# Kernel tuning notes

Hardware: AMD Instinct MI355X
Metric: run time of the kernel (lower is better)

Reference implementation:

```python
import jax, jax.numpy as jnp
import numpy as np

B, H, SQ, SK, D, INT, F = 1, 32, 2048, 2048, 128, 128, 32
THOLD = 0.5


def _mlp(x, W1, b1, W2, b2, W3, b3):
    # x: [b,h,s,d]; W*: [h,out,in] (torch Linear layout), y = x @ W^T + b, per head
    h = jax.nn.silu(jnp.einsum('bhsd,hid->bhsi', x, W1) + b1[None, :, None, :])
    h = jax.nn.silu(jnp.einsum('bhsi,hji->bhsj', h, W2) + b2[None, :, None, :])
    return jnp.einsum('bhsj,hfj->bhsf', h, W3) + b3[None, :, None, :]


def setup_inputs() -> dict:
    key = jax.random.key(0)
    ks = jax.random.split(key, 16)
    sc = 0.05  # small init so tanh stays in its linear-ish range
    inp = {
        'K': jax.random.normal(ks[0], (B, H, SK, D), jnp.float32),
        'Q': jax.random.normal(ks[1], (B, H, SQ, D), jnp.float32),
        'Wk1': jax.random.normal(ks[2], (H, INT, D), jnp.float32) * sc,
        'bk1': jax.random.normal(ks[3], (H, INT), jnp.float32) * sc,
        'Wk2': jax.random.normal(ks[4], (H, INT, INT), jnp.float32) * sc,
        'bk2': jax.random.normal(ks[5], (H, INT), jnp.float32) * sc,
        'Wk3': jax.random.normal(ks[6], (H, F, INT), jnp.float32) * sc,
        'bk3': jax.random.normal(ks[7], (H, F), jnp.float32) * sc,
        'Wq1': jax.random.normal(ks[8], (H, INT, D), jnp.float32) * sc,
        'bq1': jax.random.normal(ks[9], (H, INT), jnp.float32) * sc,
        'Wq2': jax.random.normal(ks[10], (H, INT, INT), jnp.float32) * sc,
        'bq2': jax.random.normal(ks[11], (H, INT), jnp.float32) * sc,
        'Wq3': jax.random.normal(ks[12], (H, F, INT), jnp.float32) * sc,
        'bq3': jax.random.normal(ks[13], (H, F), jnp.float32) * sc,
    }
    return inp


def reference(K, Q, Wk1, bk1, Wk2, bk2, Wk3, bk3, Wq1, bq1, Wq2, bq2, Wq3, bq3):
    # soft (hard=False) path of USA.forward
    Kl = jnp.tanh(_mlp(K, Wk1, bk1, Wk2, bk2, Wk3, bk3))  # [b,h,sk,F]
    Ql = jnp.tanh(_mlp(Q, Wq1, bq1, Wq2, bq2, Wq3, bq3))  # [b,h,sq,F]
    scores = jnp.einsum('bhtf,bhsf->bhts', Ql, Kl)        # [b,h,sq,sk]
    sq, sk = Q.shape[2], K.shape[2]
    causal = jnp.tril(jnp.ones((sq, sk), dtype=bool), k=sk - sq)
    mask_val = jnp.asarray(jnp.finfo(scores.dtype).min, scores.dtype)
    scores = jnp.where(causal[None, None], scores, mask_val)
    return jax.nn.sigmoid(scores - THOLD)
```

## Files before the change

### kernel.cpp

```cpp
#include <hip/hip_runtime.h>

#define NH  32
#define SEQ 2048
#define DIM 128
#define FD  32

typedef short          short8 __attribute__((ext_vector_type(8)));
typedef float          f32x4  __attribute__((ext_vector_type(4)));
typedef unsigned short u16x8  __attribute__((ext_vector_type(8)));

static __device__ __forceinline__ unsigned short f2bf(float f) {
    unsigned int u = __builtin_bit_cast(unsigned int, f);
    u += 0x7fffu + ((u >> 16) & 1u);
    return (unsigned short)(u >> 16);
}
static __device__ __forceinline__ float fexp(float x) {
    return __builtin_amdgcn_exp2f(x * 1.44269504088896f);
}
static __device__ __forceinline__ float sigm(float x) {
    return __builtin_amdgcn_rcpf(1.0f + fexp(-x));
}
static __device__ __forceinline__ float silu_f(float x) { return x * sigm(x); }
static __device__ __forceinline__ float tanh_f(float x) {
    return 1.0f - 2.0f * __builtin_amdgcn_rcpf(fexp(2.0f * x) + 1.0f);
}

#define WPH 36864
#define WPS (32 * WPH)

__global__ __launch_bounds__(256) void prep_weights(
    const float* __restrict__ Wk1, const float* __restrict__ Wk2,
    const float* __restrict__ Wk3, const float* __restrict__ Wq1,
    const float* __restrict__ Wq2, const float* __restrict__ Wq3,
    unsigned short* __restrict__ wimg) {
    int c = blockIdx.x * 256 + threadIdx.x;
    int s = (c >= 147456) ? 1 : 0;
    c -= s * 147456;
    const float* src;
    int dst;
    int sB = s * WPS;
    if (c < 65536) {
        int h = c >> 11, idx = c & 2047;
        int r = idx >> 4, jb = (idx & 15) * 8;
        src = (s ? Wq1 : Wk1) + h * 16384 + r * 128 + jb;
        dst = sB + h * WPH + r * 128 + (jb ^ ((r & 7) << 3));
    } else if (c < 131072) {
        int cc = c - 65536;
        int h = cc >> 11, idx = cc & 2047;
        int r = idx >> 4, jb = (idx & 15) * 8;
        src = (s ? Wq2 : Wk2) + h * 16384 + r * 128 + jb;
        dst = sB + h * WPH + 16384 + r * 128 + (jb ^ ((r & 7) << 3));
    } else {
        int cc = c - 131072;
        int h = cc >> 9, idx = cc & 511;
        int r = idx >> 4, jb = (idx & 15) * 8;
        src = (s ? Wq3 : Wk3) + h * 4096 + r * 128 + jb;
        dst = sB + h * WPH + 32768 + r * 128 + (jb ^ ((r & 7) << 3));
    }
    f32x4 u0 = *(const f32x4*)src;
    f32x4 u1 = *(const f32x4*)(src + 4);
    u16x8 p;
    p[0] = f2bf(u0[0]); p[1] = f2bf(u0[1]); p[2] = f2bf(u0[2]); p[3] = f2bf(u0[3]);
    p[4] = f2bf(u1[0]); p[5] = f2bf(u1[1]); p[6] = f2bf(u1[2]); p[7] = f2bf(u1[3]);
    *(u16x8*)(&wimg[dst]) = p;
}

template <int OT, int ACT, bool LIN>
static __device__ __forceinline__ void compute_layer(
    const short8 a[4], const unsigned short* W,
    const float* __restrict__ bias, unsigned short* dst, int lane, int wid) {
    int r0 = lane & 15, q = lane >> 4, kb = q * 8;
#pragma unroll
    for (int ot = 0; ot < OT; ++ot) {
        int wrow = ot * 16 + r0;
        int sw   = (wrow & 7) << 3;
        short8 b[4];
#pragma unroll
        for (int ks = 0; ks < 4; ++ks)
            b[ks] = *(const short8*)(&W[wrow * 128 + ((ks * 32 + kb) ^ sw)]);
        f32x4 acc = {0.f, 0.f, 0.f, 0.f};
#pragma unroll
        for (int ks = 0; ks < 4; ++ks)
            acc = __builtin_amdgcn_mfma_f32_16x16x32_bf16(a[ks], b[ks], acc, 0, 0, 0);
        float bv = bias[wrow];
#pragma unroll
        for (int r = 0; r < 4; ++r) {
            float y = acc[r] + bv;
            float v = (ACT == 0) ? silu_f(y) : tanh_f(y);
            int orow = wid * 16 + q * 4 + r;
            int ocol = ot * 16 + r0;
            if (LIN)
                dst[orow * FD + ocol] = f2bf(v);
            else
                dst[orow * 128 + (ocol ^ ((orow & 7) << 3))] = f2bf(v);
        }
    }
}

__global__ __launch_bounds__(256) void mlp_kernel(
    const float* __restrict__ K,  const float* __restrict__ Q,
    const float* __restrict__ bk1, const float* __restrict__ bk2,
    const float* __restrict__ bk3, const float* __restrict__ bq1,
    const float* __restrict__ bq2, const float* __restrict__ bq3,
    const unsigned short* __restrict__ wimg,
    unsigned short* __restrict__ Kl, unsigned short* __restrict__ Ql) {
    __shared__ unsigned short wb[128 * 128];
    __shared__ unsigned short w3[32 * 128];
    __shared__ unsigned short act[64 * 128];
    __shared__ unsigned short outb[64 * FD];
    int raw = blockIdx.x;
    int bid = (raw & 7) * 256 + (raw >> 3);
    int tb  = bid & 31;
    int h   = (bid >> 5) & 31;
    int s   = bid >> 10;

    const float* X  = s ? Q : K;
    const unsigned short* Wb = wimg + s * WPS + h * WPH;
    const float* B1 = (s ? bq1 : bk1) + h * 128;
    const float* B2 = (s ? bq2 : bk2) + h * 128;
    const float* B3 = (s ? bq3 : bk3) + h * FD;
    unsigned short* gout = (s ? Ql : Kl) + ((size_t)h * SEQ + (size_t)tb * 64) * FD;

    int tid = threadIdx.x, lane = tid & 63, wid = tid >> 6;
    int r0 = lane & 15, kb = (lane >> 4) * 8;

    const u16x8* wsrc = (const u16x8*)Wb;
#pragma unroll
    for (int i = 0; i < 8; ++i)
        *(u16x8*)(&wb[(i * 256 + tid) * 8]) = wsrc[i * 256 + tid];
    const u16x8* w3src = (const u16x8*)(Wb + 32768);
#pragma unroll
    for (int i = 0; i < 2; ++i)
        *(u16x8*)(&w3[(i * 256 + tid) * 8]) = w3src[i * 256 + tid];

    short8 a[4];
    const float* xs = X + ((size_t)h * SEQ + (size_t)tb * 64) * DIM;
    int row = wid * 16 + r0;
#pragma unroll
    for (int ks = 0; ks < 4; ++ks) {
        const float* p = xs + row * 128 + ks * 32 + kb;
        f32x4 u0 = *(const f32x4*)p;
        f32x4 u1 = *(const f32x4*)(p + 4);
        short8 t;
        t[0] = f2bf(u0[0]); t[1] = f2bf(u0[1]); t[2] = f2bf(u0[2]); t[3] = f2bf(u0[3]);
        t[4] = f2bf(u1[0]); t[5] = f2bf(u1[1]); t[6] = f2bf(u1[2]); t[7] = f2bf(u1[3]);
        a[ks] = t;
    }
    __syncthreads();
    compute_layer<8, 0, false>(a, wb, B1, act, lane, wid);
    __syncthreads();
#pragma unroll
    for (int i = 0; i < 8; ++i)
        *(u16x8*)(&wb[(i * 256 + tid) * 8]) = wsrc[2048 + i * 256 + tid];
    __syncthreads();
    {
        int sw = (row & 7) << 3;
#pragma unroll
        for (int ks = 0; ks < 4; ++ks)
            a[ks] = *(const short8*)(&act[row * 128 + ((ks * 32 + kb) ^ sw)]);
    }
    compute_layer<8, 0, false>(a, wb, B2, act, lane, wid);
    {
        int sw = (row & 7) << 3;
#pragma unroll
        for (int ks = 0; ks < 4; ++ks)
            a[ks] = *(const short8*)(&act[row * 128 + ((ks * 32 + kb) ^ sw)]);
    }
    compute_layer<2, 1, true>(a, w3, B3, outb, lane, wid);
    __syncthreads();
    *(u16x8*)(gout + tid * 8) = *(const u16x8*)(&outb[tid * 8]);
}

__global__ __launch_bounds__(256) void score_kernel(
    const unsigned short* __restrict__ Ql, const unsigned short* __restrict__ Kl,
    float* __restrict__ out) {
    int bid = blockIdx.x;
    int h   = bid >> 8;
    int tr  = (bid >> 4) & 15;
    int tc  = bid & 15;
    int tq0 = tr * 128, tk0 = tc * 128;
    int tid = threadIdx.x;
    float* ob = out + (size_t)h * SEQ * SEQ;

    if (tc > tr) {
        f32x4 z = {0.f, 0.f, 0.f, 0.f};
        for (int it = 0; it < 16; ++it) {
            int row = tq0 + it * 8 + (tid >> 5);
            int c0  = tk0 + (tid & 31) * 4;
            *(f32x4*)(ob + (size_t)row * SEQ + c0) = z;
        }
        return;
    }
    bool diag = (tc == tr);
    __shared__ float sb[4][16 * 68];
    int lane = tid & 63;
    int wid  = tid >> 6;
    int tqw  = tq0 + (wid >> 1) * 64;
    int tkw  = tk0 + (wid & 1) * 64;
    int kb   = (lane >> 4) * 8;

    short8 aq[4], bk[4];
#pragma unroll
    for (int i = 0; i < 4; ++i) {
        aq[i] = *(const short8*)(Ql + ((size_t)h * SEQ + tqw + i * 16 + (lane & 15)) * FD + kb);
        bk[i] = *(const short8*)(Kl + ((size_t)h * SEQ + tkw + i * 16 + (lane & 15)) * FD + kb);
    }
    float* my = sb[wid];
#pragma unroll
    for (int qr = 0; qr < 4; ++qr) {
#pragma unroll
        for (int ct = 0; ct < 4; ++ct) {
            f32x4 acc = {0.f, 0.f, 0.f, 0.f};
            acc = __builtin_amdgcn_mfma_f32_16x16x32_bf16(aq[qr], bk[ct], acc, 0, 0, 0);
#pragma unroll
            for (int r = 0; r < 4; ++r) {
                int lr  = (lane >> 4) * 4 + r;
                int col = ct * 16 + (lane & 15);
                float o = sigm(acc[r] - 0.5f);
                if (diag && (tkw + col) > (tqw + qr * 16 + lr)) o = 0.0f;
                my[lr * 68 + col] = o;
            }
        }
#pragma unroll
        for (int it = 0; it < 2; ++it) {
            int lr = it * 8 + (lane >> 3);
            int c0 = (lane & 7) * 8;
            f32x4 v0 = *(const f32x4*)(&my[lr * 68 + c0]);
            f32x4 v1 = *(const f32x4*)(&my[lr * 68 + c0 + 4]);
            float* dst = ob + (size_t)(tqw + qr * 16 + lr) * SEQ + tkw + c0;
            *(f32x4*)dst       = v0;
            *(f32x4*)(dst + 4) = v1;
        }
    }
}

extern "C" void kernel_launch(void* const* d_in, const int* in_sizes, int n_in,
                              void* d_out, int out_size, void* d_ws, size_t ws_size,
                              hipStream_t stream) {
    const float* K   = (const float*)d_in[0];
    const float* Q   = (const float*)d_in[1];
    const float* Wk1 = (const float*)d_in[2];
    const float* bk1 = (const float*)d_in[3];
    const float* Wk2 = (const float*)d_in[4];
    const float* bk2 = (const float*)d_in[5];
    const float* Wk3 = (const float*)d_in[6];
    const float* bk3 = (const float*)d_in[7];
    const float* Wq1 = (const float*)d_in[8];
    const float* bq1 = (const float*)d_in[9];
    const float* Wq2 = (const float*)d_in[10];
    const float* bq2 = (const float*)d_in[11];
    const float* Wq3 = (const float*)d_in[12];
    const float* bq3 = (const float*)d_in[13];

    unsigned short* Kl   = (unsigned short*)d_ws;
    unsigned short* Ql   = Kl + (size_t)NH * SEQ * FD;
    unsigned short* wimg = Ql + (size_t)NH * SEQ * FD;

    prep_weights<<<dim3(1152), dim3(256), 0, stream>>>(
        Wk1, Wk2, Wk3, Wq1, Wq2, Wq3, wimg);

    mlp_kernel<<<dim3(2 * NH * (SEQ / 64)), dim3(256), 0, stream>>>(
        K, Q, bk1, bk2, bk3, bq1, bq2, bq3, wimg, Kl, Ql);

    score_kernel<<<dim3(NH * 16 * 16), dim3(256), 0, stream>>>(
        Ql, Kl, (float*)d_out);
}
```

Before: 155.9 us.

## Hold layer-3 weights in registers; stage full-width score rows per block

Measured after the change: 139.9 us. 10.3% less time.

```diff
diff --git a/kernel.cpp b/kernel.cpp
--- a/kernel.cpp
+++ b/kernel.cpp
@@ -65,7 +65,7 @@
     *(u16x8*)(&wimg[dst]) = p;
 }
 
-template <int OT, int ACT, bool LIN>
+template <int OT, int ACT>
 static __device__ __forceinline__ void compute_layer(
     const short8 a[4], const unsigned short* W,
     const float* __restrict__ bias, unsigned short* dst, int lane, int wid) {
@@ -89,10 +89,26 @@
             float v = (ACT == 0) ? silu_f(y) : tanh_f(y);
             int orow = wid * 16 + q * 4 + r;
             int ocol = ot * 16 + r0;
-            if (LIN)
-                dst[orow * FD + ocol] = f2bf(v);
-            else
-                dst[orow * 128 + (ocol ^ ((orow & 7) << 3))] = f2bf(v);
+            dst[orow * 128 + (ocol ^ ((orow & 7) << 3))] = f2bf(v);
+        }
+    }
+}
+
+static __device__ __forceinline__ void compute_layer3_reg(
+    const short8 a[4], const short8 w3f[2][4],
+    const float* __restrict__ bias, unsigned short* dst, int lane, int wid) {
+    int r0 = lane & 15, q = lane >> 4;
+#pragma unroll
+    for (int ot = 0; ot < 2; ++ot) {
+        f32x4 acc = {0.f, 0.f, 0.f, 0.f};
+#pragma unroll
+        for (int ks = 0; ks < 4; ++ks)
+            acc = __builtin_amdgcn_mfma_f32_16x16x32_bf16(a[ks], w3f[ot][ks], acc, 0, 0, 0);
+        float bv = bias[ot * 16 + r0];
+#pragma unroll
+        for (int r = 0; r < 4; ++r) {
+            float v = tanh_f(acc[r] + bv);
+            dst[(wid * 16 + q * 4 + r) * FD + ot * 16 + r0] = f2bf(v);
         }
     }
 }
@@ -105,7 +121,6 @@
     const unsigned short* __restrict__ wimg,
     unsigned short* __restrict__ Kl, unsigned short* __restrict__ Ql) {
     __shared__ unsigned short wb[128 * 128];
-    __shared__ unsigned short w3[32 * 128];
     __shared__ unsigned short act[64 * 128];
     __shared__ unsigned short outb[64 * FD];
     int raw = blockIdx.x;
@@ -124,14 +139,21 @@
     int tid = threadIdx.x, lane = tid & 63, wid = tid >> 6;
     int r0 = lane & 15, kb = (lane >> 4) * 8;
 
+    short8 w3f[2][4];
+    {
+        const unsigned short* W3g = Wb + 32768;
+        int sw = (r0 & 7) << 3;
+#pragma unroll
+        for (int ot = 0; ot < 2; ++ot)
+#pragma unroll
+            for (int ks = 0; ks < 4; ++ks)
+                w3f[ot][ks] = *(const short8*)(&W3g[(ot * 16 + r0) * 128 + ((ks * 32 + kb) ^ sw)]);
+    }
+
     const u16x8* wsrc = (const u16x8*)Wb;
 #pragma unroll
     for (int i = 0; i < 8; ++i)
         *(u16x8*)(&wb[(i * 256 + tid) * 8]) = wsrc[i * 256 + tid];
-    const u16x8* w3src = (const u16x8*)(Wb + 32768);
-#pragma unroll
-    for (int i = 0; i < 2; ++i)
-        *(u16x8*)(&w3[(i * 256 + tid) * 8]) = w3src[i * 256 + tid];
 
     short8 a[4];
     const float* xs = X + ((size_t)h * SEQ + (size_t)tb * 64) * DIM;
@@ -147,7 +169,7 @@
         a[ks] = t;
     }
     __syncthreads();
-    compute_layer<8, 0, false>(a, wb, B1, act, lane, wid);
+    compute_layer<8, 0>(a, wb, B1, act, lane, wid);
     __syncthreads();
 #pragma unroll
     for (int i = 0; i < 8; ++i)
@@ -159,14 +181,14 @@
         for (int ks = 0; ks < 4; ++ks)
             a[ks] = *(const short8*)(&act[row * 128 + ((ks * 32 + kb) ^ sw)]);
     }
-    compute_layer<8, 0, false>(a, wb, B2, act, lane, wid);
+    compute_layer<8, 0>(a, wb, B2, act, lane, wid);
     {
         int sw = (row & 7) << 3;
 #pragma unroll
         for (int ks = 0; ks < 4; ++ks)
             a[ks] = *(const short8*)(&act[row * 128 + ((ks * 32 + kb) ^ sw)]);
     }
-    compute_layer<2, 1, true>(a, w3, B3, outb, lane, wid);
+    compute_layer3_reg(a, w3f, B3, outb, lane, wid);
     __syncthreads();
     *(u16x8*)(gout + tid * 8) = *(const u16x8*)(&outb[tid * 8]);
 }
@@ -192,44 +214,43 @@
         return;
     }
     bool diag = (tc == tr);
-    __shared__ float sb[4][16 * 68];
+    __shared__ float sb[2][16 * 130];
     int lane = tid & 63;
     int wid  = tid >> 6;
-    int tqw  = tq0 + (wid >> 1) * 64;
-    int tkw  = tk0 + (wid & 1) * 64;
+    int r0   = lane & 15;
     int kb   = (lane >> 4) * 8;
 
-    short8 aq[4], bk[4];
-#pragma unroll
-    for (int i = 0; i < 4; ++i) {
-        aq[i] = *(const short8*)(Ql + ((size_t)h * SEQ + tqw + i * 16 + (lane & 15)) * FD + kb);
-        bk[i] = *(const short8*)(Kl + ((size_t)h * SEQ + tkw + i * 16 + (lane & 15)) * FD + kb);
-    }
-    float* my = sb[wid];
-#pragma unroll
-    for (int qr = 0; qr < 4; ++qr) {
-#pragma unroll
-        for (int ct = 0; ct < 4; ++ct) {
+    short8 aq[8], bk[2];
+#pragma unroll
+    for (int i = 0; i < 8; ++i)
+        aq[i] = *(const short8*)(Ql + ((size_t)h * SEQ + tq0 + i * 16 + r0) * FD + kb);
+#pragma unroll
+    for (int ct = 0; ct < 2; ++ct)
+        bk[ct] = *(const short8*)(Kl + ((size_t)h * SEQ + tk0 + wid * 32 + ct * 16 + r0) * FD + kb);
+
+#pragma unroll
+    for (int p = 0; p < 8; ++p) {
+        float* my = sb[p & 1];
+#pragma unroll
+        for (int ct = 0; ct < 2; ++ct) {
             f32x4 acc = {0.f, 0.f, 0.f, 0.f};
-            acc = __builtin_amdgcn_mfma_f32_16x16x32_bf16(aq[qr], bk[ct], acc, 0, 0, 0);
+            acc = __builtin_amdgcn_mfma_f32_16x16x32_bf16(aq[p], bk[ct], acc, 0, 0, 0);
 #pragma unroll
             for (int r = 0; r < 4; ++r) {
                 int lr  = (lane >> 4) * 4 + r;
-                int col = ct * 16 + (lane & 15);
+                int col = wid * 32 + ct * 16 + r0;
                 float o = sigm(acc[r] - 0.5f);
-                if (diag && (tkw + col) > (tqw + qr * 16 + lr)) o = 0.0f;
-                my[lr * 68 + col] = o;
+                if (diag && (tk0 + col) > (tq0 + p * 16 + lr)) o = 0.0f;
+                my[lr * 130 + col] = o;
             }
         }
-#pragma unroll
-        for (int it = 0; it < 2; ++it) {
-            int lr = it * 8 + (lane >> 3);
-            int c0 = (lane & 7) * 8;
-            f32x4 v0 = *(const f32x4*)(&my[lr * 68 + c0]);
-            f32x4 v1 = *(const f32x4*)(&my[lr * 68 + c0 + 4]);
-            float* dst = ob + (size_t)(tqw + qr * 16 + lr) * SEQ + tkw + c0;
-            *(f32x4*)dst       = v0;
-            *(f32x4*)(dst + 4) = v1;
+        __syncthreads();
+#pragma unroll
+        for (int j = 0; j < 2; ++j) {
+            int row = (tid >> 5) + j * 8;
+            int c0  = (tid & 31) * 4;
+            f32x4 v = *(const f32x4*)(&my[row * 130 + c0]);
+            *(f32x4*)(ob + (size_t)(tq0 + p * 16 + row) * SEQ + tk0 + c0) = v;
         }
     }
 }
```
